# Performance work log

Hardware: AMD Instinct MI355X
Metric: run time of the kernel (lower is better)

Reference implementation:

```python
import jax, jax.numpy as jnp
import numpy as np
import math
from jax import lax

SQRT_HALF = math.sqrt(0.5)

def _causal_dilated_conv(x, w, b, dilation):
    # x: [B, C, T], w: [O, I, K] (torch layout), causal left padding (K-1)*dilation
    k = w.shape[-1]
    pad = (k - 1) * dilation
    y = lax.conv_general_dilated(
        x, w,
        window_strides=(1,),
        padding=((pad, 0),),
        rhs_dilation=(dilation,),
        dimension_numbers=('NCH', 'OIH', 'NCH'),
    )
    return y + b[None, :, None]


def setup_inputs() -> dict:
    key = jax.random.key(0)
    ks = jax.random.split(key, 9)
    B, C, S, T, K = 8, 512, 256, 8192, 2
    scale = 1.0 / np.sqrt(C * K)
    return {
        'x': jax.random.normal(ks[0], (B, C, T), jnp.float32),
        'filter_w': jax.random.normal(ks[1], (C, C, K), jnp.float32) * scale,
        'filter_b': jax.random.normal(ks[2], (C,), jnp.float32) * scale,
        'gate_w': jax.random.normal(ks[3], (C, C, K), jnp.float32) * scale,
        'gate_b': jax.random.normal(ks[4], (C,), jnp.float32) * scale,
        'res_w': jax.random.normal(ks[5], (C, C), jnp.float32) / np.sqrt(C),
        'res_b': jax.random.normal(ks[6], (C,), jnp.float32) / np.sqrt(C),
        'skip_w': jax.random.normal(ks[7], (S, C), jnp.float32) / np.sqrt(C),
        'skip_b': jax.random.normal(ks[8], (S,), jnp.float32) / np.sqrt(C),
        'dilation': 4,
    }


def reference(x, filter_w, filter_b, gate_w, gate_b, res_w, res_b, skip_w, skip_b, dilation):
    filter_out = jnp.tanh(_causal_dilated_conv(x, filter_w, filter_b, dilation))
    gate_out = jax.nn.sigmoid(_causal_dilated_conv(x, gate_w, gate_b, dilation))
    x_gated = filter_out * gate_out  # [B, C, T]
    # 1x1 convs as channel contractions
    res_out = jnp.einsum('oc,bct->bot', res_w, x_gated) + res_b[None, :, None]
    skip_out = jnp.einsum('sc,bct->bst', skip_w, x_gated) + skip_b[None, :, None]
    return ((x + res_out) * SQRT_HALF, skip_out)
```

## Files before the change

kernel.cpp:

```cpp
#include <hip/hip_runtime.h>
#include <hip/hip_bf16.h>

typedef __attribute__((ext_vector_type(4))) float f32x4;
typedef __attribute__((ext_vector_type(8))) short bf16x8;
typedef unsigned int   u32;
typedef unsigned short u16;

#define DPAD 8
#define B_   8
#define C_   512
#define T_   8192
#define S_   256

#define OFF_WBIG 0u
#define OFF_W2   2097152u
#define OFF_B1   2883584u
#define OFF_B2   2887680u
#define OFF_XT   2891776u
#define OFF_ZT   70066176u

__device__ __forceinline__ u16 f2bf(float f) {
  u32 u = __builtin_bit_cast(u32, f);
  u += 0x7FFFu + ((u >> 16) & 1u);
  return (u16)(u >> 16);
}
__device__ __forceinline__ float sigm_(float x) { return 1.0f / (1.0f + __expf(-x)); }
__device__ __forceinline__ float tanh_(float x) { return 2.0f / (1.0f + __expf(-2.0f * x)) - 1.0f; }

__device__ __forceinline__ void gload_lds16(const void* g, void* l) {
  __builtin_amdgcn_global_load_lds(
      (const __attribute__((address_space(1))) void*)g,
      (__attribute__((address_space(3))) void*)l, 16, 0, 0);
}

__global__ void pack_kernel(const float* __restrict__ fw, const float* __restrict__ fb,
                            const float* __restrict__ gw, const float* __restrict__ gb,
                            const float* __restrict__ rw, const float* __restrict__ rb,
                            const float* __restrict__ sw, const float* __restrict__ sb,
                            u16* __restrict__ Wbig, u16* __restrict__ W2,
                            float* __restrict__ b1, float* __restrict__ b2,
                            u16* __restrict__ Xt)
{
  int idx = blockIdx.x * 256 + threadIdx.x;
  if (idx < 1048576) {
    int row = idx >> 10, k = idx & 1023;
    int i = row >> 1;
    const float* src = (row & 1) ? gw : fw;
    float v = src[((i << 9) + (k & 511)) * 2 + ((k < 512) ? 1 : 0)];
    Wbig[idx] = f2bf(v);
    return;
  }
  idx -= 1048576;
  if (idx < 393216) {
    int r = idx >> 9, k = idx & 511;
    float v = (r < 512) ? rw[(r << 9) + k] : sw[((r - 512) << 9) + k];
    W2[idx] = f2bf(v);
    return;
  }
  idx -= 393216;
  if (idx < 1024) { b1[idx] = (idx & 1) ? gb[idx >> 1] : fb[idx >> 1]; return; }
  idx -= 1024;
  if (idx < 768) { b2[idx] = (idx < 512) ? rb[idx] : sb[idx - 512]; return; }
  idx -= 768;
  if (idx < B_ * DPAD * C_) {
    int b = idx >> 12;
    int rest = idx & 4095;
    Xt[(size_t)b * (T_ + DPAD) * C_ + rest] = 0;
  }
}

__global__ __launch_bounds__(256) void transpose_kernel(const float* __restrict__ x,
                                                        u16* __restrict__ Xt)
{
  __shared__ float tile[64][65];
  int bid = blockIdx.x;
  int ct = bid & 7, tt = (bid >> 3) & 127, b = bid >> 10;
  int w = threadIdx.x >> 6, ln = threadIdx.x & 63;
  const float* xp = x + ((size_t)(b * C_ + ct * 64)) * T_ + tt * 64;
#pragma unroll
  for (int r = 0; r < 16; ++r) {
    int cl = r * 4 + w;
    tile[cl][ln] = xp[(size_t)cl * T_ + ln];
  }
  __syncthreads();
  u16* op = Xt + ((size_t)b * (T_ + DPAD) + DPAD + tt * 64) * C_ + ct * 64;
#pragma unroll
  for (int r = 0; r < 16; ++r) {
    int tl = r * 4 + w;
    op[(size_t)tl * C_ + ln] = f2bf(tile[ln][tl]);
  }
}

__global__ __launch_bounds__(256, 2) void gemm1_kernel(
    const u16* __restrict__ W, const u16* __restrict__ Xt,
    const float* __restrict__ b1, u16* __restrict__ Zt,
    const int* __restrict__ dptr)
{
  __shared__ __align__(16) u16 As[128 * 32];
  __shared__ __align__(16) u16 Bs[128 * 32];
  const int d = *dptr;
  const int tid = threadIdx.x;
  const int lane = tid & 63, wave = tid >> 6;
  const int wm = wave >> 1, wn = wave & 1;

  const int bid = blockIdx.x;
  const int xcd = bid & 7;
  const int idx = bid >> 3;
  const int mt  = idx & 7;
  const int nt  = (xcd << 6) | (idx >> 3);
  const int m0 = mt * 128;
  const int n0g = nt * 128;
  const int b = n0g >> 13, t0 = n0g & (T_ - 1);
  const int srow = tid >> 2;
  const int skk  = (tid & 3) * 8;

  f32x4 acc[4][4];
#pragma unroll
  for (int i = 0; i < 4; ++i)
#pragma unroll
    for (int j = 0; j < 4; ++j) acc[i][j] = (f32x4){0.f, 0.f, 0.f, 0.f};

  const int aoff = (wm * 64 + (lane & 15)) * 32 + (lane >> 4) * 8;
  const int boff = (wn * 64 + (lane & 15)) * 32 + (lane >> 4) * 8;
  const size_t xtb = (size_t)b * (T_ + DPAD) * C_;

  for (int kc = 0; kc < 32; ++kc) {
    const int k = kc * 32 + skk;
    const int col = k & 511;
    const int rsh = (k >= 512) ? d : 0;
    const u16* gA = W + (size_t)(m0 + srow) * 1024 + k;
    const u16* gB = Xt + xtb + (size_t)(DPAD + t0 + srow - rsh) * C_ + col;
    gload_lds16(gA,             As + tid * 8);
    gload_lds16(gA + 64 * 1024, As + 2048 + tid * 8);
    gload_lds16(gB,             Bs + tid * 8);
    gload_lds16(gB + 64 * C_,   Bs + 2048 + tid * 8);
    asm volatile("s_waitcnt vmcnt(0)" ::: "memory");
    __syncthreads();
    bf16x8 af[4], bfr[4];
#pragma unroll
    for (int i = 0; i < 4; ++i) af[i]  = *(const bf16x8*)(As + aoff + i * 512);
#pragma unroll
    for (int j = 0; j < 4; ++j) bfr[j] = *(const bf16x8*)(Bs + boff + j * 512);
#pragma unroll
    for (int i = 0; i < 4; ++i)
#pragma unroll
      for (int j = 0; j < 4; ++j)
        acc[i][j] = __builtin_amdgcn_mfma_f32_16x16x32_bf16(af[i], bfr[j], acc[i][j], 0, 0, 0);
    __syncthreads();
  }

#pragma unroll
  for (int i = 0; i < 4; ++i) {
    const int R = m0 + wm * 64 + i * 16 + ((lane >> 4) << 2);
    const float bi0 = b1[R], bi1 = b1[R + 1], bi2 = b1[R + 2], bi3 = b1[R + 3];
    const int c0 = R >> 1;
#pragma unroll
    for (int j = 0; j < 4; ++j) {
      const int ttc = t0 + wn * 64 + j * 16 + (lane & 15);
      f32x4 v = acc[i][j];
      float z0 = tanh_(v[0] + bi0) * sigm_(v[1] + bi1);
      float z1 = tanh_(v[2] + bi2) * sigm_(v[3] + bi3);
      u32 p = (u32)f2bf(z0) | ((u32)f2bf(z1) << 16);
      *(u32*)(Zt + (size_t)(b * T_ + ttc) * C_ + c0) = p;
    }
  }
}

__global__ __launch_bounds__(256, 4) void gemm2_kernel(
    const u16* __restrict__ W2, const u16* __restrict__ Zt,
    const float* __restrict__ b2, const float* __restrict__ x,
    float* __restrict__ out)
{
  __shared__ __align__(16) u16 As[128 * 32];
  __shared__ __align__(16) u16 Bs[128 * 32];
  __shared__ __align__(16) float fstall[4 * 1088];
  const int tid = threadIdx.x;
  const int lane = tid & 63, wave = tid >> 6;
  const int wm = wave >> 1, wn = wave & 1;

  const int bid = blockIdx.x;
  const int xcd = bid & 7;
  const int idx = bid >> 3;
  const int mt  = idx % 6;
  const int nt  = (xcd << 6) + idx / 6;
  const int m0 = mt * 128;
  const int n0g = nt * 128;
  const int b = n0g >> 13, t0 = n0g & (T_ - 1);
  const int srow = tid >> 2;
  const int skk  = (tid & 3) * 8;

  f32x4 acc[4][4];
#pragma unroll
  for (int i = 0; i < 4; ++i)
#pragma unroll
    for (int j = 0; j < 4; ++j) acc[i][j] = (f32x4){0.f, 0.f, 0.f, 0.f};

  const int aoff = (wm * 64 + (lane & 15)) * 32 + (lane >> 4) * 8;
  const int boff = (wn * 64 + (lane & 15)) * 32 + (lane >> 4) * 8;
  const size_t ztb = (size_t)b * T_ * C_;

  for (int kc = 0; kc < 16; ++kc) {
    const int k = kc * 32 + skk;
    const u16* gA = W2 + (size_t)(m0 + srow) * 512 + k;
    const u16* gB = Zt + ztb + (size_t)(t0 + srow) * C_ + k;
    gload_lds16(gA,            As + tid * 8);
    gload_lds16(gA + 64 * 512, As + 2048 + tid * 8);
    gload_lds16(gB,            Bs + tid * 8);
    gload_lds16(gB + 64 * C_,  Bs + 2048 + tid * 8);
    asm volatile("s_waitcnt vmcnt(0)" ::: "memory");
    __syncthreads();
    bf16x8 af[4], bfr[4];
#pragma unroll
    for (int i = 0; i < 4; ++i) af[i]  = *(const bf16x8*)(As + aoff + i * 512);
#pragma unroll
    for (int j = 0; j < 4; ++j) bfr[j] = *(const bf16x8*)(Bs + boff + j * 512);
#pragma unroll
    for (int i = 0; i < 4; ++i)
#pragma unroll
      for (int j = 0; j < 4; ++j)
        acc[i][j] = __builtin_amdgcn_mfma_f32_16x16x32_bf16(af[i], bfr[j], acc[i][j], 0, 0, 0);
    __syncthreads();
  }

  float* const fst = fstall + wave * 1088;
  const int g = lane >> 4, p = lane & 15;
  const bool isres = (m0 < 512);

#pragma unroll
  for (int i = 0; i < 4; ++i) {
#pragma unroll
    for (int j = 0; j < 4; ++j)
#pragma unroll
      for (int r = 0; r < 4; ++r)
        fst[(g * 4 + r) * 68 + j * 16 + p] = acc[i][j][r];
#pragma unroll
    for (int q = 0; q < 4; ++q) {
      const int lrow = q * 4 + g;
      const int row = m0 + wm * 64 + i * 16 + lrow;
      const int t = t0 + wn * 64 + p * 4;
      f32x4 v = *(const f32x4*)&fst[lrow * 68 + p * 4];
      const float bias = b2[row];
      f32x4 res;
      if (isres) {
        const size_t o = ((size_t)(b * 512 + row)) * T_ + t;
        f32x4 xv = *(const f32x4*)(x + o);
#pragma unroll
        for (int e = 0; e < 4; ++e)
          res[e] = (xv[e] + v[e] + bias) * 0.70710678118654752f;
        *(f32x4*)(out + o) = res;
      } else {
        const size_t o = (size_t)33554432 + ((size_t)(b * 256 + (row - 512))) * T_ + t;
#pragma unroll
        for (int e = 0; e < 4; ++e)
          res[e] = v[e] + bias;
        *(f32x4*)(out + o) = res;
      }
    }
  }
}

extern "C" void kernel_launch(void* const* d_in, const int* in_sizes, int n_in,
                              void* d_out, int out_size, void* d_ws, size_t ws_size,
                              hipStream_t stream) {
  const float* x  = (const float*)d_in[0];
  const float* fw = (const float*)d_in[1];
  const float* fb = (const float*)d_in[2];
  const float* gw = (const float*)d_in[3];
  const float* gb = (const float*)d_in[4];
  const float* rw = (const float*)d_in[5];
  const float* rb = (const float*)d_in[6];
  const float* sw = (const float*)d_in[7];
  const float* sb = (const float*)d_in[8];
  const int* dil  = (const int*)d_in[9];

  char* ws = (char*)d_ws;
  u16*   Wbig = (u16*)(ws + OFF_WBIG);
  u16*   W2   = (u16*)(ws + OFF_W2);
  float* b1   = (float*)(ws + OFF_B1);
  float* b2   = (float*)(ws + OFF_B2);
  u16*   Xt   = (u16*)(ws + OFF_XT);
  u16*   Zt   = (u16*)(ws + OFF_ZT);
  float* out  = (float*)d_out;

  hipLaunchKernelGGL(pack_kernel, dim3(5767), dim3(256), 0, stream,
                     fw, fb, gw, gb, rw, rb, sw, sb, Wbig, W2, b1, b2, Xt);
  hipLaunchKernelGGL(transpose_kernel, dim3(8192), dim3(256), 0, stream, x, Xt);
  hipLaunchKernelGGL(gemm1_kernel, dim3(4096), dim3(256), 0, stream, Wbig, Xt, b1, Zt, dil);
  hipLaunchKernelGGL(gemm2_kernel, dim3(3072), dim3(256), 0, stream, W2, Zt, b2, x, out);
}
```

Measured before the change: 334.8 us.

## Restructure gemm1 into 256x256 tiles with double-buffered swizzled LDS pipeline

Gemm1 moves from 128x128 tiles with a single LDS buffer and 4 waves to 256x256 tiles with 8 waves, K-steps of 64, and a two-stage double-buffered asynchronous global-to-LDS pipeline that waits with vmcnt(8). LDS columns are XOR-swizzled to avoid bank conflicts, and setprio is raised around the MFMA bursts. The aim is to hide load latency and raise arithmetic intensity per byte loaded. In exchange it uses 128KB of LDS and 128 accumulator registers per thread, which may limit occupancy. The grid drops to 1024 blocks.

```diff
diff --git a/kernel.cpp b/kernel.cpp
--- a/kernel.cpp
+++ b/kernel.cpp
@@ -91,79 +91,105 @@
   }
 }
 
-__global__ __launch_bounds__(256, 2) void gemm1_kernel(
+__global__ __launch_bounds__(512, 2) void gemm1_kernel(
     const u16* __restrict__ W, const u16* __restrict__ Xt,
     const float* __restrict__ b1, u16* __restrict__ Zt,
     const int* __restrict__ dptr)
 {
-  __shared__ __align__(16) u16 As[128 * 32];
-  __shared__ __align__(16) u16 Bs[128 * 32];
-  const int d = *dptr;
+  __shared__ __align__(16) u16 smem[4 * 16384];
+  const int dcap = *dptr;
   const int tid = threadIdx.x;
   const int lane = tid & 63, wave = tid >> 6;
-  const int wm = wave >> 1, wn = wave & 1;
+  const int wm = wave >> 2, wn = wave & 3;
 
   const int bid = blockIdx.x;
   const int xcd = bid & 7;
   const int idx = bid >> 3;
-  const int mt  = idx & 7;
-  const int nt  = (xcd << 6) | (idx >> 3);
-  const int m0 = mt * 128;
-  const int n0g = nt * 128;
+  const int mt  = idx & 3;
+  const int nt  = (xcd << 5) | (idx >> 2);
+  const int m0  = mt * 256;
+  const int n0g = nt * 256;
   const int b = n0g >> 13, t0 = n0g & (T_ - 1);
-  const int srow = tid >> 2;
-  const int skk  = (tid & 3) * 8;
-
-  f32x4 acc[4][4];
-#pragma unroll
-  for (int i = 0; i < 4; ++i)
+
+  const int row0 = tid >> 3;
+  const int ksw  = (((tid & 7) ^ (row0 & 7)) << 3);
+  const size_t xtb = (size_t)b * (T_ + DPAD) * C_;
+
+  f32x4 acc[8][4];
+#pragma unroll
+  for (int i = 0; i < 8; ++i)
 #pragma unroll
     for (int j = 0; j < 4; ++j) acc[i][j] = (f32x4){0.f, 0.f, 0.f, 0.f};
 
-  const int aoff = (wm * 64 + (lane & 15)) * 32 + (lane >> 4) * 8;
-  const int boff = (wn * 64 + (lane & 15)) * 32 + (lane >> 4) * 8;
-  const size_t xtb = (size_t)b * (T_ + DPAD) * C_;
-
-  for (int kc = 0; kc < 32; ++kc) {
-    const int k = kc * 32 + skk;
-    const int col = k & 511;
-    const int rsh = (k >= 512) ? d : 0;
-    const u16* gA = W + (size_t)(m0 + srow) * 1024 + k;
-    const u16* gB = Xt + xtb + (size_t)(DPAD + t0 + srow - rsh) * C_ + col;
-    gload_lds16(gA,             As + tid * 8);
-    gload_lds16(gA + 64 * 1024, As + 2048 + tid * 8);
-    gload_lds16(gB,             Bs + tid * 8);
-    gload_lds16(gB + 64 * C_,   Bs + 2048 + tid * 8);
-    asm volatile("s_waitcnt vmcnt(0)" ::: "memory");
-    __syncthreads();
-    bf16x8 af[4], bfr[4];
-#pragma unroll
-    for (int i = 0; i < 4; ++i) af[i]  = *(const bf16x8*)(As + aoff + i * 512);
-#pragma unroll
-    for (int j = 0; j < 4; ++j) bfr[j] = *(const bf16x8*)(Bs + boff + j * 512);
-#pragma unroll
-    for (int i = 0; i < 4; ++i)
-#pragma unroll
-      for (int j = 0; j < 4; ++j)
-        acc[i][j] = __builtin_amdgcn_mfma_f32_16x16x32_bf16(af[i], bfr[j], acc[i][j], 0, 0, 0);
-    __syncthreads();
-  }
-
-#pragma unroll
-  for (int i = 0; i < 4; ++i) {
-    const int R = m0 + wm * 64 + i * 16 + ((lane >> 4) << 2);
+#define STAGE1(kt_, dd) do {                                                   \
+    const int kglob_ = (kt_) * 64 + ksw;                                       \
+    const int col_ = kglob_ & 511;                                             \
+    const int rsh_ = (kglob_ >= 512) ? dcap : 0;                               \
+    const u16* gA_ = W + (size_t)(m0 + row0) * 1024 + kglob_;                  \
+    const u16* gB_ = Xt + xtb + (size_t)(DPAD + t0 + row0 - rsh_) * C_ + col_; \
+    u16* As_ = smem + (dd) * 16384;                                            \
+    u16* Bs_ = smem + 32768 + (dd) * 16384;                                    \
+    _Pragma("unroll") for (int r_ = 0; r_ < 4; ++r_) {                         \
+      gload_lds16(gA_ + (size_t)r_ * 64 * 1024, As_ + r_ * 4096 + tid * 8);    \
+      gload_lds16(gB_ + (size_t)r_ * 64 * C_,   Bs_ + r_ * 4096 + tid * 8);    \
+    }                                                                          \
+  } while (0)
+
+#define COMPUTE1(dd) do {                                                      \
+    const u16* Ab_ = smem + (dd) * 16384;                                      \
+    const u16* Bb_ = smem + 32768 + (dd) * 16384;                              \
+    _Pragma("unroll") for (int s_ = 0; s_ < 2; ++s_) {                         \
+      const int blk_ = ((s_ * 4 + (lane >> 4)) ^ (lane & 7)) * 8;              \
+      bf16x8 af_[8], bf_[4];                                                   \
+      _Pragma("unroll") for (int i_ = 0; i_ < 8; ++i_)                         \
+        af_[i_] = *(const bf16x8*)(Ab_ + (wm * 128 + i_ * 16 + (lane & 15)) * 64 + blk_); \
+      _Pragma("unroll") for (int j_ = 0; j_ < 4; ++j_)                         \
+        bf_[j_] = *(const bf16x8*)(Bb_ + (wn * 64 + j_ * 16 + (lane & 15)) * 64 + blk_);  \
+      __builtin_amdgcn_s_setprio(1);                                           \
+      _Pragma("unroll") for (int i_ = 0; i_ < 8; ++i_)                         \
+        _Pragma("unroll") for (int j_ = 0; j_ < 4; ++j_)                       \
+          acc[i_][j_] = __builtin_amdgcn_mfma_f32_16x16x32_bf16(af_[i_], bf_[j_], acc[i_][j_], 0, 0, 0); \
+      __builtin_amdgcn_s_setprio(0);                                           \
+    }                                                                          \
+  } while (0)
+
+  STAGE1(0, 0);
+  STAGE1(1, 1);
+  for (int it = 0; it < 15; ++it) {
+    asm volatile("s_waitcnt vmcnt(8)" ::: "memory");
+    __builtin_amdgcn_sched_barrier(0);
+    __builtin_amdgcn_s_barrier();
+    __builtin_amdgcn_sched_barrier(0);
+    COMPUTE1(it & 1);
+    __builtin_amdgcn_sched_barrier(0);
+    __builtin_amdgcn_s_barrier();
+    __builtin_amdgcn_sched_barrier(0);
+    if (it < 14) STAGE1(it + 2, it & 1);
+  }
+  asm volatile("s_waitcnt vmcnt(0)" ::: "memory");
+  __builtin_amdgcn_sched_barrier(0);
+  __builtin_amdgcn_s_barrier();
+  __builtin_amdgcn_sched_barrier(0);
+  COMPUTE1(1);
+
+  const int g = lane >> 4, p = lane & 15;
+#pragma unroll
+  for (int i = 0; i < 8; ++i) {
+    const int R = m0 + wm * 128 + i * 16 + (g << 2);
     const float bi0 = b1[R], bi1 = b1[R + 1], bi2 = b1[R + 2], bi3 = b1[R + 3];
     const int c0 = R >> 1;
 #pragma unroll
     for (int j = 0; j < 4; ++j) {
-      const int ttc = t0 + wn * 64 + j * 16 + (lane & 15);
+      const int ttc = t0 + wn * 64 + j * 16 + p;
       f32x4 v = acc[i][j];
       float z0 = tanh_(v[0] + bi0) * sigm_(v[1] + bi1);
       float z1 = tanh_(v[2] + bi2) * sigm_(v[3] + bi3);
-      u32 p = (u32)f2bf(z0) | ((u32)f2bf(z1) << 16);
-      *(u32*)(Zt + (size_t)(b * T_ + ttc) * C_ + c0) = p;
+      u32 pk = (u32)f2bf(z0) | ((u32)f2bf(z1) << 16);
+      *(u32*)(Zt + (size_t)(b * T_ + ttc) * C_ + c0) = pk;
     }
   }
+#undef STAGE1
+#undef COMPUTE1
 }
 
 __global__ __launch_bounds__(256, 4) void gemm2_kernel(
@@ -285,6 +311,6 @@
   hipLaunchKernelGGL(pack_kernel, dim3(5767), dim3(256), 0, stream,
                      fw, fb, gw, gb, rw, rb, sw, sb, Wbig, W2, b1, b2, Xt);
   hipLaunchKernelGGL(transpose_kernel, dim3(8192), dim3(256), 0, stream, x, Xt);
-  hipLaunchKernelGGL(gemm1_kernel, dim3(4096), dim3(256), 0, stream, Wbig, Xt, b1, Zt, dil);
+  hipLaunchKernelGGL(gemm1_kernel, dim3(1024), dim3(512), 0, stream, Wbig, Xt, b1, Zt, dil);
   hipLaunchKernelGGL(gemm2_kernel, dim3(3072), dim3(256), 0, stream, W2, Zt, b2, x, out);
 }
```

After: 317.3 us. -5.2%, faster.

## Widen gemm1 K-tile to 64 with XOR-swizzled LDS and vectorize transpose stores

Applied to the files above, without the earlier changes.

gemm1 now stages 64-wide K tiles (halving the loop iterations and barrier count) into LDS laid out with an XOR swizzle, so MFMA fragment reads avoid bank conflicts. The launch bound is raised to 4 blocks per CU. The transpose kernel now writes four bf16 values per store instead of one. LDS per block doubles to 32 KB, which may limit occupancy, and there is still no double buffering.

```diff
diff --git a/kernel.cpp b/kernel.cpp
--- a/kernel.cpp
+++ b/kernel.cpp
@@ -3,6 +3,7 @@
 
 typedef __attribute__((ext_vector_type(4))) float f32x4;
 typedef __attribute__((ext_vector_type(8))) short bf16x8;
+typedef __attribute__((ext_vector_type(4))) unsigned short u16x4;
 typedef unsigned int   u32;
 typedef unsigned short u16;
 
@@ -84,35 +85,43 @@
   }
   __syncthreads();
   u16* op = Xt + ((size_t)b * (T_ + DPAD) + DPAD + tt * 64) * C_ + ct * 64;
-#pragma unroll
-  for (int r = 0; r < 16; ++r) {
-    int tl = r * 4 + w;
-    op[(size_t)tl * C_ + ln] = f2bf(tile[ln][tl]);
-  }
-}
-
-__global__ __launch_bounds__(256, 2) void gemm1_kernel(
+  const int q = threadIdx.x & 15;
+  const int cr = threadIdx.x >> 4;
+#pragma unroll
+  for (int r = 0; r < 4; ++r) {
+    const int tl = r * 16 + cr;
+    u16x4 v;
+#pragma unroll
+    for (int e = 0; e < 4; ++e) v[e] = f2bf(tile[q * 4 + e][tl]);
+    *(u16x4*)(op + (size_t)tl * C_ + q * 4) = v;
+  }
+}
+
+__global__ __launch_bounds__(256, 4) void gemm1_kernel(
     const u16* __restrict__ W, const u16* __restrict__ Xt,
     const float* __restrict__ b1, u16* __restrict__ Zt,
     const int* __restrict__ dptr)
 {
-  __shared__ __align__(16) u16 As[128 * 32];
-  __shared__ __align__(16) u16 Bs[128 * 32];
-  const int d = *dptr;
+  __shared__ __align__(16) u16 As[8192];
+  __shared__ __align__(16) u16 Bs[8192];
+  const int dcap = *dptr;
   const int tid = threadIdx.x;
   const int lane = tid & 63, wave = tid >> 6;
   const int wm = wave >> 1, wn = wave & 1;
+  const int lp = lane & 15, lg = lane >> 4, lx = lane & 7;
 
   const int bid = blockIdx.x;
   const int xcd = bid & 7;
   const int idx = bid >> 3;
   const int mt  = idx & 7;
   const int nt  = (xcd << 6) | (idx >> 3);
-  const int m0 = mt * 128;
+  const int m0  = mt * 128;
   const int n0g = nt * 128;
   const int b = n0g >> 13, t0 = n0g & (T_ - 1);
-  const int srow = tid >> 2;
-  const int skk  = (tid & 3) * 8;
+  const size_t xtb = (size_t)b * (T_ + DPAD) * C_;
+
+  const int srl = tid >> 3;
+  const int sxk = ((tid & 7) ^ (srl & 7)) << 3;
 
   f32x4 acc[4][4];
 #pragma unroll
@@ -120,50 +129,62 @@
 #pragma unroll
     for (int j = 0; j < 4; ++j) acc[i][j] = (f32x4){0.f, 0.f, 0.f, 0.f};
 
-  const int aoff = (wm * 64 + (lane & 15)) * 32 + (lane >> 4) * 8;
-  const int boff = (wn * 64 + (lane & 15)) * 32 + (lane >> 4) * 8;
-  const size_t xtb = (size_t)b * (T_ + DPAD) * C_;
-
-  for (int kc = 0; kc < 32; ++kc) {
-    const int k = kc * 32 + skk;
-    const int col = k & 511;
-    const int rsh = (k >= 512) ? d : 0;
-    const u16* gA = W + (size_t)(m0 + srow) * 1024 + k;
-    const u16* gB = Xt + xtb + (size_t)(DPAD + t0 + srow - rsh) * C_ + col;
-    gload_lds16(gA,             As + tid * 8);
-    gload_lds16(gA + 64 * 1024, As + 2048 + tid * 8);
-    gload_lds16(gB,             Bs + tid * 8);
-    gload_lds16(gB + 64 * C_,   Bs + 2048 + tid * 8);
+#define SQA1(kt_, q_) gload_lds16(                                             \
+    W + (size_t)(m0 + (q_) * 32 + srl) * 1024 + (kt_) * 64 + sxk,              \
+    As + (q_) * 2048 + tid * 8)
+
+#define SQB1(kt_, q_) do {                                                     \
+    const int rsh_ = ((kt_) >= 8) ? dcap : 0;                                  \
+    const int col_ = (((kt_) & 7) << 6) + sxk;                                 \
+    gload_lds16(Xt + xtb + (size_t)(DPAD + t0 + (q_) * 32 + srl - rsh_) * C_ + col_, \
+                Bs + (q_) * 2048 + tid * 8);                                   \
+  } while (0)
+
+#define LDA1(f_, kk_) \
+  (*(const bf16x8*)(As + (size_t)(wm * 64 + (f_) * 16 + lp) * 64 + ((((kk_) * 4 + lg) ^ lx) << 3)))
+#define LDB1(j_, kk_) \
+  (*(const bf16x8*)(Bs + (size_t)(wn * 64 + (j_) * 16 + lp) * 64 + ((((kk_) * 4 + lg) ^ lx) << 3)))
+
+  for (int kt = 0; kt < 16; ++kt) {
+    SQA1(kt, 0); SQA1(kt, 1); SQA1(kt, 2); SQA1(kt, 3);
+    SQB1(kt, 0); SQB1(kt, 1); SQB1(kt, 2); SQB1(kt, 3);
     asm volatile("s_waitcnt vmcnt(0)" ::: "memory");
     __syncthreads();
-    bf16x8 af[4], bfr[4];
-#pragma unroll
-    for (int i = 0; i < 4; ++i) af[i]  = *(const bf16x8*)(As + aoff + i * 512);
-#pragma unroll
-    for (int j = 0; j < 4; ++j) bfr[j] = *(const bf16x8*)(Bs + boff + j * 512);
-#pragma unroll
-    for (int i = 0; i < 4; ++i)
-#pragma unroll
-      for (int j = 0; j < 4; ++j)
-        acc[i][j] = __builtin_amdgcn_mfma_f32_16x16x32_bf16(af[i], bfr[j], acc[i][j], 0, 0, 0);
+    bf16x8 af[4][2], bfr[4][2];
+#pragma unroll
+    for (int i = 0; i < 4; ++i) { af[i][0] = LDA1(i, 0); af[i][1] = LDA1(i, 1); }
+#pragma unroll
+    for (int j = 0; j < 4; ++j) { bfr[j][0] = LDB1(j, 0); bfr[j][1] = LDB1(j, 1); }
+#pragma unroll
+    for (int kk = 0; kk < 2; ++kk)
+#pragma unroll
+      for (int i = 0; i < 4; ++i)
+#pragma unroll
+        for (int j = 0; j < 4; ++j)
+          acc[i][j] = __builtin_amdgcn_mfma_f32_16x16x32_bf16(af[i][kk], bfr[j][kk], acc[i][j], 0, 0, 0);
     __syncthreads();
   }
 
+  const int g4 = lane >> 4, p = lane & 15;
 #pragma unroll
   for (int i = 0; i < 4; ++i) {
-    const int R = m0 + wm * 64 + i * 16 + ((lane >> 4) << 2);
+    const int R = m0 + wm * 64 + i * 16 + (g4 << 2);
     const float bi0 = b1[R], bi1 = b1[R + 1], bi2 = b1[R + 2], bi3 = b1[R + 3];
     const int c0 = R >> 1;
 #pragma unroll
     for (int j = 0; j < 4; ++j) {
-      const int ttc = t0 + wn * 64 + j * 16 + (lane & 15);
+      const int ttc = t0 + wn * 64 + j * 16 + p;
       f32x4 v = acc[i][j];
       float z0 = tanh_(v[0] + bi0) * sigm_(v[1] + bi1);
       float z1 = tanh_(v[2] + bi2) * sigm_(v[3] + bi3);
-      u32 p = (u32)f2bf(z0) | ((u32)f2bf(z1) << 16);
-      *(u32*)(Zt + (size_t)(b * T_ + ttc) * C_ + c0) = p;
+      u32 pk = (u32)f2bf(z0) | ((u32)f2bf(z1) << 16);
+      *(u32*)(Zt + (size_t)(b * T_ + ttc) * C_ + c0) = pk;
     }
   }
+#undef SQA1
+#undef SQB1
+#undef LDA1
+#undef LDB1
 }
 
 __global__ __launch_bounds__(256, 4) void gemm2_kernel(
```

Measured after the change: 311.0 us. 1.08x faster.
